# Kernel optimization log

Hardware: AMD Instinct MI355X
Metric: run time of the kernel (lower is better)

The kernel has to match this reference:

```python
import jax, jax.numpy as jnp
import numpy as np

V_MIN = -10.0
V_MAX = 10.0
NUM_ATOMS = 51
DISCOUNT = 0.99
BS = 524288


def setup_inputs() -> dict:
    key = jax.random.key(0)
    k1, k2, k3 = jax.random.split(key, 3)
    reward = jax.random.normal(k1, (BS, 1), dtype=jnp.float32)
    probs = jax.random.uniform(k2, (BS, NUM_ATOMS), dtype=jnp.float32)
    probs = probs / jnp.sum(probs, axis=-1, keepdims=True)  # valid distribution
    not_done = jnp.round(jax.random.uniform(k3, (BS, 1), dtype=jnp.float32))
    return {"reward": reward, "probs": probs, "not_done": not_done}


def reference(reward, probs, not_done):
    bs = probs.shape[0]
    atom_delta = (V_MAX - V_MIN) / (NUM_ATOMS - 1)
    atom_values = V_MIN + atom_delta * jnp.arange(NUM_ATOMS, dtype=jnp.float32)  # [A]
    # Bellman-shifted atom positions, clipped to support
    new_atom_values = reward + DISCOUNT * not_done * atom_values[None, :]  # [bs, A]
    new_atom_values = jnp.clip(new_atom_values, V_MIN, V_MAX)
    b = (new_atom_values - V_MIN) / atom_delta  # fractional atom index
    l = jnp.floor(b)
    u = jnp.ceil(b)
    d_m_l = (u + (l == u).astype(probs.dtype) - b) * probs
    d_m_u = (b - l) * probs
    li = l.astype(jnp.int32)
    ui = u.astype(jnp.int32)
    rows = jnp.arange(bs, dtype=jnp.int32)[:, None]  # [bs,1] broadcasts over atoms
    new_probs = (
        jnp.zeros_like(probs)
        .at[rows, li].add(d_m_l)
        .at[rows, ui].add(d_m_u)
    )
    return new_probs
```

## Files before the change

### kernel.cpp

```cpp
#include <hip/hip_runtime.h>


#define NUM_ATOMS 51
#define ROWS_PER_WAVE 16
#define WAVES_PER_BLOCK 4
#define ROWS_PER_BLOCK (ROWS_PER_WAVE * WAVES_PER_BLOCK)
#define TILE_FLOATS (ROWS_PER_BLOCK * NUM_ATOMS)
#define QUARTER_FLOATS (ROWS_PER_WAVE * NUM_ATOMS)
#define QUARTER_V4 (QUARTER_FLOATS / 4)

#define WAVE_FENCE() do { __builtin_amdgcn_wave_barrier(); \
                          asm volatile("" ::: "memory"); } while (0)

__global__ __launch_bounds__(256, 8) void catproj_kernel(
    const float* __restrict__ reward,
    const float* __restrict__ probs,
    const float* __restrict__ not_done,
    float* __restrict__ out)
{
    __shared__ __align__(16) float lds[TILE_FLOATS];

    const int tid  = threadIdx.x;
    const int wave = tid >> 6;
    const int lane = tid & 63;
    const int qrow = lane >> 2;
    const int seg  = lane & 3;

    const int row   = blockIdx.x * ROWS_PER_BLOCK + wave * ROWS_PER_WAVE + qrow;
    const int gbase = blockIdx.x * TILE_FLOATS + wave * QUARTER_FLOATS;

    float* __restrict__ q = lds + wave * QUARTER_FLOATS;

    const float4* __restrict__ g4 = (const float4*)(probs + gbase);
    float4* __restrict__ q4 = (float4*)q;
#pragma unroll
    for (int k = 0; k < 3; ++k) q4[k * 64 + lane] = g4[k * 64 + lane];
    if (lane < QUARTER_V4 - 192) q4[192 + lane] = g4[192 + lane];

    const float r  = reward[row];
    const float nd = not_done[row];
    WAVE_FENCE();

    float* __restrict__ myrow = q + qrow * NUM_ATOMS;
    const int a0 = seg * 13;
    float p[13];
#pragma unroll
    for (int i = 0; i < 12; ++i) p[i] = myrow[a0 + i];
    p[12] = (seg < 3) ? myrow[a0 + 12] : 0.0f;
    WAVE_FENCE();

    const float4 z4 = make_float4(0.f, 0.f, 0.f, 0.f);
#pragma unroll
    for (int k = 0; k < 3; ++k) q4[k * 64 + lane] = z4;
    if (lane < QUARTER_V4 - 192) q4[192 + lane] = z4;
    WAVE_FENCE();

    const float c     = 0.99f * nd;
    const float base2 = fmaf(-25.f, c, fmaf(2.5f, r, 25.f));
    const float b0    = fminf(fmaxf(fmaf(c, (float)a0, base2), 0.f), 50.f);
    float curf = floorf(b0);
    float* dst = myrow + (int)curf;
    float accL = 0.f, accU = 0.f;
#pragma unroll
    for (int i = 0; i < 13; ++i) {
        const int a = a0 + i;
        float b = fmaf(c, (float)a, base2);
        b = fminf(fmaxf(b, 0.f), 50.f);
        const float lf = floorf(b);
        const float pa = p[i];
        const float mu = (b - lf) * pa;
        const float ml = pa - mu;
        if (lf != curf) {
            *dst = accL;
            ++dst;
            accL = accU;
            accU = 0.f;
            curf = lf;
        }
        accL += ml;
        accU += mu;
    }

    asm volatile("" ::: "memory");
#pragma unroll
    for (int s = 0; s < 4; ++s) {
        if (seg == s) {
            dst[0] += accL;
            if (curf < 50.f) dst[1] += accU;
        }
        asm volatile("" ::: "memory");
    }
    WAVE_FENCE();

    float4* __restrict__ o4 = (float4*)(out + gbase);
#pragma unroll
    for (int k = 0; k < 3; ++k) o4[k * 64 + lane] = q4[k * 64 + lane];
    if (lane < QUARTER_V4 - 192) o4[192 + lane] = q4[192 + lane];
}

extern "C" void kernel_launch(void* const* d_in, const int* in_sizes, int n_in,
                              void* d_out, int out_size, void* d_ws, size_t ws_size,
                              hipStream_t stream) {
    const float* reward   = (const float*)d_in[0];
    const float* probs    = (const float*)d_in[1];
    const float* not_done = (const float*)d_in[2];
    float* out = (float*)d_out;

    const int bs = in_sizes[0];
    const int grid = bs / ROWS_PER_BLOCK;
    catproj_kernel<<<grid, 256, 0, stream>>>(reward, probs, not_done, out);
}
```

Baseline: 195.9 us.

## Process four tiles per block with register prefetch of the next tile

Each block now loops over four consecutive 64-row tiles instead of one. The next tile's probs, reward and not_done loads are issued into registers before the current tile is computed, so global load latency overlaps with the LDS scatter work. The grid shrinks by four, which cuts block launch overhead but leaves fewer blocks to hide latency and adds register pressure.

```diff
diff --git a/kernel.cpp b/kernel.cpp
--- a/kernel.cpp
+++ b/kernel.cpp
@@ -8,6 +8,7 @@
 #define TILE_FLOATS (ROWS_PER_BLOCK * NUM_ATOMS)
 #define QUARTER_FLOATS (ROWS_PER_WAVE * NUM_ATOMS)
 #define QUARTER_V4 (QUARTER_FLOATS / 4)
+#define TILES_PER_BLOCK 4
 
 #define WAVE_FENCE() do { __builtin_amdgcn_wave_barrier(); \
                           asm volatile("" ::: "memory"); } while (0)
@@ -26,76 +27,108 @@
     const int qrow = lane >> 2;
     const int seg  = lane & 3;
 
-    const int row   = blockIdx.x * ROWS_PER_BLOCK + wave * ROWS_PER_WAVE + qrow;
-    const int gbase = blockIdx.x * TILE_FLOATS + wave * QUARTER_FLOATS;
-
-    float* __restrict__ q = lds + wave * QUARTER_FLOATS;
-
-    const float4* __restrict__ g4 = (const float4*)(probs + gbase);
+    float* __restrict__ q  = lds + wave * QUARTER_FLOATS;
     float4* __restrict__ q4 = (float4*)q;
-#pragma unroll
-    for (int k = 0; k < 3; ++k) q4[k * 64 + lane] = g4[k * 64 + lane];
-    if (lane < QUARTER_V4 - 192) q4[192 + lane] = g4[192 + lane];
-
-    const float r  = reward[row];
-    const float nd = not_done[row];
-    WAVE_FENCE();
-
     float* __restrict__ myrow = q + qrow * NUM_ATOMS;
     const int a0 = seg * 13;
-    float p[13];
-#pragma unroll
-    for (int i = 0; i < 12; ++i) p[i] = myrow[a0 + i];
-    p[12] = (seg < 3) ? myrow[a0 + 12] : 0.0f;
-    WAVE_FENCE();
 
-    const float4 z4 = make_float4(0.f, 0.f, 0.f, 0.f);
-#pragma unroll
-    for (int k = 0; k < 3; ++k) q4[k * 64 + lane] = z4;
-    if (lane < QUARTER_V4 - 192) q4[192 + lane] = z4;
-    WAVE_FENCE();
+    int gq   = blockIdx.x * TILES_PER_BLOCK * TILE_FLOATS + wave * QUARTER_FLOATS;
+    int grow = blockIdx.x * TILES_PER_BLOCK * ROWS_PER_BLOCK
+             + wave * ROWS_PER_WAVE + qrow;
 
-    const float c     = 0.99f * nd;
-    const float base2 = fmaf(-25.f, c, fmaf(2.5f, r, 25.f));
-    const float b0    = fminf(fmaxf(fmaf(c, (float)a0, base2), 0.f), 50.f);
-    float curf = floorf(b0);
-    float* dst = myrow + (int)curf;
-    float accL = 0.f, accU = 0.f;
-#pragma unroll
-    for (int i = 0; i < 13; ++i) {
-        const int a = a0 + i;
-        float b = fmaf(c, (float)a, base2);
-        b = fminf(fmaxf(b, 0.f), 50.f);
-        const float lf = floorf(b);
-        const float pa = p[i];
-        const float mu = (b - lf) * pa;
-        const float ml = pa - mu;
-        if (lf != curf) {
-            *dst = accL;
-            ++dst;
-            accL = accU;
-            accU = 0.f;
-            curf = lf;
-        }
-        accL += ml;
-        accU += mu;
+    float4 f0, f1, f2, f3;
+    float pr, pnd;
+    {
+        const float4* __restrict__ g4 = (const float4*)(probs + gq);
+        f0 = g4[lane];
+        f1 = g4[64 + lane];
+        f2 = g4[128 + lane];
+        f3 = (lane < 12) ? g4[192 + lane] : make_float4(0.f, 0.f, 0.f, 0.f);
+        pr  = reward[grow];
+        pnd = not_done[grow];
     }
 
-    asm volatile("" ::: "memory");
 #pragma unroll
-    for (int s = 0; s < 4; ++s) {
-        if (seg == s) {
-            dst[0] += accL;
-            if (curf < 50.f) dst[1] += accU;
+    for (int t = 0; t < TILES_PER_BLOCK; ++t) {
+        const int out_base = gq;
+        const float r  = pr;
+        const float nd = pnd;
+
+        q4[lane]       = f0;
+        q4[64 + lane]  = f1;
+        q4[128 + lane] = f2;
+        if (lane < 12) q4[192 + lane] = f3;
+
+        if (t + 1 < TILES_PER_BLOCK) {
+            gq   += TILE_FLOATS;
+            grow += ROWS_PER_BLOCK;
+            const float4* __restrict__ g4 = (const float4*)(probs + gq);
+            f0 = g4[lane];
+            f1 = g4[64 + lane];
+            f2 = g4[128 + lane];
+            if (lane < 12) f3 = g4[192 + lane];
+            pr  = reward[grow];
+            pnd = not_done[grow];
         }
+        WAVE_FENCE();
+
+        float p[13];
+#pragma unroll
+        for (int i = 0; i < 12; ++i) p[i] = myrow[a0 + i];
+        p[12] = (seg < 3) ? myrow[a0 + 12] : 0.0f;
+        WAVE_FENCE();
+
+        const float4 z4 = make_float4(0.f, 0.f, 0.f, 0.f);
+        q4[lane]       = z4;
+        q4[64 + lane]  = z4;
+        q4[128 + lane] = z4;
+        if (lane < 12) q4[192 + lane] = z4;
+        WAVE_FENCE();
+
+        const float c     = 0.99f * nd;
+        const float base2 = fmaf(-25.f, c, fmaf(2.5f, r, 25.f));
+        const float b0    = fminf(fmaxf(fmaf(c, (float)a0, base2), 0.f), 50.f);
+        float curf = floorf(b0);
+        float* dst = myrow + (int)curf;
+        float accL = 0.f, accU = 0.f;
+#pragma unroll
+        for (int i = 0; i < 13; ++i) {
+            const int a = a0 + i;
+            float b = fmaf(c, (float)a, base2);
+            b = fminf(fmaxf(b, 0.f), 50.f);
+            const float lf = floorf(b);
+            const float pa = p[i];
+            const float mu = (b - lf) * pa;
+            const float ml = pa - mu;
+            if (lf != curf) {
+                *dst = accL;
+                ++dst;
+                accL = accU;
+                accU = 0.f;
+                curf = lf;
+            }
+            accL += ml;
+            accU += mu;
+        }
+
         asm volatile("" ::: "memory");
+#pragma unroll
+        for (int s = 0; s < 4; ++s) {
+            if (seg == s) {
+                dst[0] += accL;
+                if (curf < 50.f) dst[1] += accU;
+            }
+            asm volatile("" ::: "memory");
+        }
+        WAVE_FENCE();
+
+        float4* __restrict__ o4 = (float4*)(out + out_base);
+        o4[lane]       = q4[lane];
+        o4[64 + lane]  = q4[64 + lane];
+        o4[128 + lane] = q4[128 + lane];
+        if (lane < 12) o4[192 + lane] = q4[192 + lane];
+        WAVE_FENCE();
     }
-    WAVE_FENCE();
-
-    float4* __restrict__ o4 = (float4*)(out + gbase);
-#pragma unroll
-    for (int k = 0; k < 3; ++k) o4[k * 64 + lane] = q4[k * 64 + lane];
-    if (lane < QUARTER_V4 - 192) o4[192 + lane] = q4[192 + lane];
 }
 
 extern "C" void kernel_launch(void* const* d_in, const int* in_sizes, int n_in,
@@ -107,6 +140,6 @@
     float* out = (float*)d_out;
 
     const int bs = in_sizes[0];
-    const int grid = bs / ROWS_PER_BLOCK;
+    const int grid = bs / (ROWS_PER_BLOCK * TILES_PER_BLOCK);
     catproj_kernel<<<grid, 256, 0, stream>>>(reward, probs, not_done, out);
 }
```

Measured after the change: 206.9 us. +5.6%, slower.
